# Kernel tuning notes

Measured on AMD Instinct MI355X. Metric: run time of the kernel, lower is better.

The kernel has to match this reference:

```python
import jax, jax.numpy as jnp
import numpy as np

B, S, D, H, HD, F = 2, 2048, 1024, 16, 64, 4096
EPS = 1e-5


def layer_norm(x, g, b):
    m = jnp.mean(x, axis=-1, keepdims=True)
    v = jnp.var(x, axis=-1, keepdims=True)
    return (x - m) * jax.lax.rsqrt(v + EPS) * g + b


def setup_inputs() -> dict:
    key = jax.random.key(0)
    ks = jax.random.split(key, 8)
    hidden_states = jax.random.normal(ks[0], (B, S, D), dtype=jnp.float32)
    # additive causal mask: 0 where allowed, -1e9 where masked
    causal = jnp.tril(jnp.ones((S, S), dtype=bool))
    attention_mask = jnp.where(causal, 0.0, -1e9).astype(jnp.float32)[None, None]
    sd = 1.0 / np.sqrt(D)
    Wq = jax.random.normal(ks[1], (D, D), jnp.float32) * sd
    Wk = jax.random.normal(ks[2], (D, D), jnp.float32) * sd
    Wv = jax.random.normal(ks[3], (D, D), jnp.float32) * sd
    Wo = jax.random.normal(ks[4], (D, D), jnp.float32) * sd
    W1 = jax.random.normal(ks[5], (D, F), jnp.float32) * sd
    W2 = jax.random.normal(ks[6], (F, D), jnp.float32) * (1.0 / np.sqrt(F))
    ln1_g = jnp.ones((D,), jnp.float32)
    ln1_b = jnp.zeros((D,), jnp.float32)
    ln2_g = jnp.ones((D,), jnp.float32)
    ln2_b = jnp.zeros((D,), jnp.float32)
    return dict(hidden_states=hidden_states, attention_mask=attention_mask,
                ln1_g=ln1_g, ln1_b=ln1_b, Wq=Wq, Wk=Wk, Wv=Wv, Wo=Wo,
                ln2_g=ln2_g, ln2_b=ln2_b, W1=W1, W2=W2)


def reference(hidden_states, attention_mask, ln1_g, ln1_b, Wq, Wk, Wv, Wo,
              ln2_g, ln2_b, W1, W2):
    x = hidden_states
    # --- attention sublayer (pre-LN) ---
    h = layer_norm(x, ln1_g, ln1_b)
    q = (h @ Wq).reshape(B, S, H, HD).transpose(0, 2, 1, 3)  # b h s d
    k = (h @ Wk).reshape(B, S, H, HD).transpose(0, 2, 1, 3)
    v = (h @ Wv).reshape(B, S, H, HD).transpose(0, 2, 1, 3)
    scores = jnp.einsum('bhqd,bhkd->bhqk', q, k) / np.sqrt(HD)
    scores = scores + attention_mask
    attn = jax.nn.softmax(scores, axis=-1)
    ctx = jnp.einsum('bhqk,bhkd->bhqd', attn, v)
    ctx = ctx.transpose(0, 2, 1, 3).reshape(B, S, D)
    x = x + ctx @ Wo
    # --- FFN sublayer (pre-LN) ---
    h = layer_norm(x, ln2_g, ln2_b)
    h = jax.nn.gelu(h @ W1, approximate=False) @ W2
    out = x + h
    return out, k, v
```

## Files before the change

### kernel.cpp

```cpp
#include <hip/hip_runtime.h>
#include <hip/hip_bf16.h>
#include <cstdint>
#include <cstddef>

#define BB 2
#define SS 2048
#define DD 1024
#define HH 16
#define HDIM 64
#define FF 4096
#define RR (BB*SS)

typedef __attribute__((ext_vector_type(8))) short short8;
typedef __attribute__((ext_vector_type(4))) float floatx4;

__device__ __forceinline__ unsigned short f2bf(float f){
    __hip_bfloat16 h = __float2bfloat16(f);
    return *reinterpret_cast<unsigned short*>(&h);
}

__device__ __forceinline__ void load_lds16(const void* g, void* l){
    __builtin_amdgcn_global_load_lds((__attribute__((address_space(1))) void*)g,
                                     (__attribute__((address_space(3))) void*)l, 16, 0, 0);
}


template<int BN, int EPI>
__global__ __launch_bounds__(256) void gemm_bt(const unsigned short* __restrict__ A,
                                               const unsigned short* __restrict__ B,
                                               int M, int N, int K, int KS,
                                               float* __restrict__ cf,
                                               const float* __restrict__ resid,
                                               unsigned short* __restrict__ cbf,
                                               unsigned short* __restrict__ qb,
                                               float* __restrict__ kout,
                                               unsigned short* __restrict__ kbf,
                                               float* __restrict__ vout)
{
    constexpr int MI_M = (BN==128) ? 4 : 2;
    __shared__ __align__(16) unsigned short As[2][128*64];
    __shared__ __align__(16) unsigned short Bs[2][BN*64];
    const int tid  = threadIdx.x;
    const int lane = tid & 63;
    const int wave = tid >> 6;
    const int quad = lane >> 4, l15 = lane & 15;
    const int wrow = (BN==128) ? (wave>>1)*64 : wave*32;
    const int wcol = (BN==128) ? (wave&1)*64 : 0;

    const unsigned gx = gridDim.x;
    const unsigned nwg = gx * gridDim.y;
    const unsigned bid = blockIdx.y * gx + blockIdx.x;
    const unsigned cpx = nwg >> 3;
    const unsigned swz = (bid & 7) * cpx + (bid >> 3);
    const int bx = (int)(swz % gx), by = (int)(swz / gx);

    const int gm0 = by * 128, gn0 = bx * BN;
    const int k0 = blockIdx.z * KS;
    const int niter = KS >> 6;
    const int phase = (int)((unsigned)(bx + by) % (unsigned)niter);

    floatx4 acc[MI_M][4];
#pragma unroll
    for (int i=0;i<MI_M;i++)
#pragma unroll
        for (int j=0;j<4;j++) acc[i][j] = (floatx4){0.f,0.f,0.f,0.f};

    const int rsub = lane >> 3;
    const int d8   = (lane & 7) * 8;
    const int ksub = ((lane & 7) ^ rsub) * 8;
    constexpr int nchw = (128 + BN) / 32;

    auto stage = [&](int kt, int buf){
#pragma unroll
        for (int i=0;i<nchw;i++){
            int c = wave*nchw + i;
            if (c < 16)
                load_lds16(A + (size_t)(gm0 + c*8 + rsub)*K + kt + ksub,
                           &As[buf][c*512 + rsub*64 + d8]);
            else
                load_lds16(B + (size_t)(gn0 + (c-16)*8 + rsub)*K + kt + ksub,
                           &Bs[buf][(c-16)*512 + rsub*64 + d8]);
        }
    };

    stage(k0 + phase*64, 0);
    int cur = 0;
    for (int it=0; it<niter; it++){
        __syncthreads();
        if (it+1 < niter){
            int j = it + 1 + phase; if (j >= niter) j -= niter;
            stage(k0 + j*64, cur^1);
        }
        const unsigned short* as = As[cur];
        const unsigned short* bs = Bs[cur];
#pragma unroll
        for (int kk=0; kk<64; kk+=32){
            const int cb4 = kk >> 3;
            short8 af[MI_M], bfr[4];
#pragma unroll
            for (int mi=0;mi<MI_M;mi++){
                int row = wrow + mi*16 + l15;
                af[mi] = *(const short8*)&as[row*64 + (((cb4+quad) ^ (row&7)))*8];
            }
#pragma unroll
            for (int ni=0;ni<4;ni++){
                int row = wcol + ni*16 + l15;
                bfr[ni] = *(const short8*)&bs[row*64 + (((cb4+quad) ^ (row&7)))*8];
            }
#pragma unroll
            for (int mi=0;mi<MI_M;mi++)
#pragma unroll
                for (int ni=0;ni<4;ni++)
                    acc[mi][ni] = __builtin_amdgcn_mfma_f32_16x16x32_bf16(af[mi], bfr[ni], acc[mi][ni], 0, 0, 0);
        }
        cur ^= 1;
    }

#pragma unroll
    for (int mi=0;mi<MI_M;mi++)
#pragma unroll
        for (int ni=0;ni<4;ni++)
#pragma unroll
            for (int r=0;r<4;r++){
                int row = gm0 + wrow + mi*16 + quad*4 + r;
                int col = gn0 + wcol + ni*16 + l15;
                float v = acc[mi][ni][r];
                if constexpr (EPI == 1){
                    int region = gn0 >> 10;
                    if (region == 0){
                        qb[(size_t)row*1024 + col] = f2bf(v);
                    } else {
                        int c1 = col & 1023;
                        int h = c1 >> 6, d = c1 & 63;
                        int b = row >> 11, s = row & (SS-1);
                        size_t o = ((size_t)((b*HH + h)*SS + s))*HDIM + d;
                        if (region == 1){ kout[o] = v; kbf[o] = f2bf(v); }
                        else            { vout[o] = v; }
                    }
                } else if constexpr (EPI == 2){
                    size_t o = (size_t)row*N + col;
                    cf[o] = v + resid[o];
                } else if constexpr (EPI == 3){
                    float u = v*(0.79788456f + 0.0356774081f*v*v);
                    float g = v / (1.f + exp2f(-2.88539008f*u));
                    cbf[(size_t)row*N + col] = f2bf(g);
                } else {
                    cf[(size_t)blockIdx.z*M*N + (size_t)row*N + col] = v;
                }
            }
}

__global__ __launch_bounds__(256) void combine2_kernel(const float* __restrict__ p0,
                                                       const float* __restrict__ p1,
                                                       const float* __restrict__ resid,
                                                       float* __restrict__ out, int n4)
{
    const int i = blockIdx.x*256 + threadIdx.x;
    if (i >= n4) return;
    float4 a = ((const float4*)p0)[i];
    float4 b = ((const float4*)p1)[i];
    float4 c = ((const float4*)resid)[i];
    ((float4*)out)[i] = make_float4(a.x+b.x+c.x, a.y+b.y+c.y, a.z+b.z+c.z, a.w+b.w+c.w);
}

__global__ __launch_bounds__(256) void attn_kernel(const unsigned short* __restrict__ qbf,
                                                   const unsigned short* __restrict__ kbf,
                                                   const unsigned short* __restrict__ vtbf,
                                                   unsigned short* __restrict__ ctx)
{
    __shared__ unsigned short Ks[2][64*64];
    __shared__ unsigned short Vs[2][64*64];
    __shared__ unsigned short Ps[4][16*64];
    const int tid  = threadIdx.x;
    const int lane = tid & 63;
    const int wave = tid >> 6;
    const int quad = lane >> 4, l15 = lane & 15;
    const int aqt = blockIdx.x;
    const int bqt = 31 - aqt;
    const int bh = blockIdx.y;
    const int b = bh >> 4, h = bh & 15;
    const int q0a = aqt * 64, q0b = bqt * 64;

    const unsigned short* kb  = kbf  + (size_t)bh * SS * HDIM;
    const unsigned short* vtb = vtbf + (size_t)bh * HDIM * SS;

    const unsigned short* qra = qbf + (size_t)(b*SS + q0a + wave*16 + l15)*DD + h*HDIM + quad*8;
    const unsigned short* qrb = qbf + (size_t)(b*SS + q0b + wave*16 + l15)*DD + h*HDIM + quad*8;
    short8 qa0 = *(const short8*)qra;
    short8 qa1 = *(const short8*)(qra + 32);
    short8 qb0 = *(const short8*)qrb;
    short8 qb1 = *(const short8*)(qrb + 32);

    float lpA[4] = {0.f,0.f,0.f,0.f}, lpB[4] = {0.f,0.f,0.f,0.f};
    floatx4 accA[4], accB[4];
#pragma unroll
    for (int n=0;n<4;n++){ accA[n] = (floatx4){0.f,0.f,0.f,0.f}; accB[n] = (floatx4){0.f,0.f,0.f,0.f}; }

    const int r8 = lane >> 3;
    const int c8 = ((lane & 7) ^ r8) * 8;
    const int d8 = (lane & 7) * 8;
    const int nkt = bqt + 1;
    const float SC = 0.125f * 1.44269504f;

#pragma unroll
    for (int p=0;p<2;p++){
        int row = p*32 + wave*8 + r8;
        load_lds16(kb  + (size_t)row*HDIM + c8,  &Ks[0][row*64 + d8]);
        load_lds16(vtb + (size_t)row*SS   + c8,  &Vs[0][row*64 + d8]);
    }

    unsigned short* pl = Ps[wave];
    int cur = 0;
    for (int kt=0; kt<nkt; kt++){
        __syncthreads();
        if (kt+1 < nkt){
            int nb = cur ^ 1;
#pragma unroll
            for (int p=0;p<2;p++){
                int row = p*32 + wave*8 + r8;
                load_lds16(kb  + (size_t)((kt+1)*64 + row)*HDIM + c8, &Ks[nb][row*64 + d8]);
                load_lds16(vtb + (size_t)row*SS + (size_t)(kt+1)*64 + c8, &Vs[nb][row*64 + d8]);
            }
        }
        const unsigned short* ks = Ks[cur];
        const unsigned short* vs = Vs[cur];

        short8 kf0[4], kf1[4];
#pragma unroll
        for (int j=0;j<4;j++){
            int row = j*16 + l15;
            kf0[j] = *(const short8*)&ks[row*64 + ((quad     ^ (row&7)))*8];
            kf1[j] = *(const short8*)&ks[row*64 + (((quad+4) ^ (row&7)))*8];
        }
        short8 vf0[4], vf1[4];
#pragma unroll
        for (int n=0;n<4;n++){
            int row = n*16 + l15;
            vf0[n] = *(const short8*)&vs[row*64 + ((quad     ^ (row&7)))*8];
            vf1[n] = *(const short8*)&vs[row*64 + (((quad+4) ^ (row&7)))*8];
        }

        {
            floatx4 s[4];
            __builtin_amdgcn_s_setprio(1);
#pragma unroll
            for (int j=0;j<4;j++){
                floatx4 zz = (floatx4){0.f,0.f,0.f,0.f};
                zz = __builtin_amdgcn_mfma_f32_16x16x32_bf16(qb0, kf0[j], zz, 0, 0, 0);
                zz = __builtin_amdgcn_mfma_f32_16x16x32_bf16(qb1, kf1[j], zz, 0, 0, 0);
                s[j] = zz;
            }
            __builtin_amdgcn_s_setprio(0);
#pragma unroll
            for (int j=0;j<4;j++)
#pragma unroll
                for (int r=0;r<4;r++){
                    int prow = quad*4 + r;
                    float p = exp2f(s[j][r]*SC);
                    if (kt == bqt){
                        int row = q0b + wave*16 + prow;
                        int col = kt*64 + j*16 + l15;
                        if (col > row) p = 0.f;
                    }
                    lpB[r] += p;
                    int ch = (2*j + (l15>>3)) ^ (prow&7);
                    pl[prow*64 + ch*8 + (l15&7)] = f2bf(p);
                }
            short8 pf0 = *(const short8*)&pl[l15*64 + ((quad     ^ (l15&7)))*8];
            short8 pf1 = *(const short8*)&pl[l15*64 + (((quad+4) ^ (l15&7)))*8];
            __builtin_amdgcn_s_setprio(1);
#pragma unroll
            for (int n=0;n<4;n++){
                accB[n] = __builtin_amdgcn_mfma_f32_16x16x32_bf16(pf0, vf0[n], accB[n], 0, 0, 0);
                accB[n] = __builtin_amdgcn_mfma_f32_16x16x32_bf16(pf1, vf1[n], accB[n], 0, 0, 0);
            }
            __builtin_amdgcn_s_setprio(0);
        }

        if (kt <= aqt){
            floatx4 s[4];
            __builtin_amdgcn_s_setprio(1);
#pragma unroll
            for (int j=0;j<4;j++){
                floatx4 zz = (floatx4){0.f,0.f,0.f,0.f};
                zz = __builtin_amdgcn_mfma_f32_16x16x32_bf16(qa0, kf0[j], zz, 0, 0, 0);
                zz = __builtin_amdgcn_mfma_f32_16x16x32_bf16(qa1, kf1[j], zz, 0, 0, 0);
                s[j] = zz;
            }
            __builtin_amdgcn_s_setprio(0);
#pragma unroll
            for (int j=0;j<4;j++)
#pragma unroll
                for (int r=0;r<4;r++){
                    int prow = quad*4 + r;
                    float p = exp2f(s[j][r]*SC);
                    if (kt == aqt){
                        int row = q0a + wave*16 + prow;
                        int col = kt*64 + j*16 + l15;
                        if (col > row) p = 0.f;
                    }
                    lpA[r] += p;
                    int ch = (2*j + (l15>>3)) ^ (prow&7);
                    pl[prow*64 + ch*8 + (l15&7)] = f2bf(p);
                }
            short8 pf0 = *(const short8*)&pl[l15*64 + ((quad     ^ (l15&7)))*8];
            short8 pf1 = *(const short8*)&pl[l15*64 + (((quad+4) ^ (l15&7)))*8];
            __builtin_amdgcn_s_setprio(1);
#pragma unroll
            for (int n=0;n<4;n++){
                accA[n] = __builtin_amdgcn_mfma_f32_16x16x32_bf16(pf0, vf0[n], accA[n], 0, 0, 0);
                accA[n] = __builtin_amdgcn_mfma_f32_16x16x32_bf16(pf1, vf1[n], accA[n], 0, 0, 0);
            }
            __builtin_amdgcn_s_setprio(0);
        }
        cur ^= 1;
    }

#pragma unroll
    for (int r=0;r<4;r++){
        float va = lpA[r], vb = lpB[r];
        va += __shfl_xor(va, 1); vb += __shfl_xor(vb, 1);
        va += __shfl_xor(va, 2); vb += __shfl_xor(vb, 2);
        va += __shfl_xor(va, 4); vb += __shfl_xor(vb, 4);
        va += __shfl_xor(va, 8); vb += __shfl_xor(vb, 8);
        lpA[r] = va; lpB[r] = vb;
    }
#pragma unroll
    for (int n=0;n<4;n++)
#pragma unroll
        for (int r=0;r<4;r++){
            float oa = accA[n][r] / lpA[r];
            float ob = accB[n][r] / lpB[r];
            ctx[(size_t)(b*SS + q0a + wave*16 + quad*4 + r)*DD + h*HDIM + n*16 + l15] = f2bf(oa);
            ctx[(size_t)(b*SS + q0b + wave*16 + quad*4 + r)*DD + h*HDIM + n*16 + l15] = f2bf(ob);
        }
}

__global__ __launch_bounds__(256) void ln_kernel(const float* __restrict__ x,
                                                 const float* __restrict__ g,
                                                 const float* __restrict__ bparm,
                                                 unsigned short* __restrict__ out)
{
    __shared__ float red[8];
    const int row = blockIdx.x;
    const int tid = threadIdx.x;
    const float* xr = x + (size_t)row*DD;
    float4 v = *(const float4*)(xr + tid*4);
    float s  = v.x+v.y+v.z+v.w;
    float sq = v.x*v.x + v.y*v.y + v.z*v.z + v.w*v.w;
#pragma unroll
    for (int off=1; off<64; off<<=1){ s += __shfl_xor(s, off); sq += __shfl_xor(sq, off); }
    if ((tid & 63) == 0){ red[tid>>6] = s; red[4 + (tid>>6)] = sq; }
    __syncthreads();
    float ts = red[0]+red[1]+red[2]+red[3];
    float tq = red[4]+red[5]+red[6]+red[7];
    float mean = ts * (1.f/DD);
    float var  = tq * (1.f/DD) - mean*mean;
    float inv  = rsqrtf(var + 1e-5f);
    float4 gv = *(const float4*)(g + tid*4);
    float4 bv = *(const float4*)(bparm + tid*4);
    ushort4 o;
    o.x = f2bf((v.x-mean)*inv*gv.x + bv.x);
    o.y = f2bf((v.y-mean)*inv*gv.y + bv.y);
    o.z = f2bf((v.z-mean)*inv*gv.z + bv.z);
    o.w = f2bf((v.w-mean)*inv*gv.w + bv.w);
    *(ushort4*)(out + (size_t)row*DD + tid*4) = o;
}

__global__ __launch_bounds__(256) void castT_kernel(const float* __restrict__ in,
                                                    unsigned short* __restrict__ out,
                                                    int R, int C)
{
    __shared__ float t[32][33];
    const size_t zoff = (size_t)blockIdx.z * R * C;
    in  += zoff; out += zoff;
    const int tr = blockIdx.y*32, tc = blockIdx.x*32;
    const int lr = threadIdx.x >> 5, lc = threadIdx.x & 31;
#pragma unroll
    for (int i=0;i<4;i++)
        t[lr + i*8][lc] = in[(size_t)(tr + lr + i*8)*C + tc + lc];
    __syncthreads();
#pragma unroll
    for (int i=0;i<4;i++)
        out[(size_t)(tc + lr + i*8)*R + tr + lc] = f2bf(t[lc][lr + i*8]);
}

__global__ __launch_bounds__(256) void castT4_kernel(const float* __restrict__ i0,
                                                     const float* __restrict__ i1,
                                                     const float* __restrict__ i2,
                                                     const float* __restrict__ i3,
                                                     unsigned short* __restrict__ o0,
                                                     unsigned short* __restrict__ o1,
                                                     unsigned short* __restrict__ o2,
                                                     unsigned short* __restrict__ o3)
{
    __shared__ float t[32][33];
    const int z = blockIdx.z;
    const float* in = (z==0) ? i0 : (z==1) ? i1 : (z==2) ? i2 : i3;
    unsigned short* out = (z==0) ? o0 : (z==1) ? o1 : (z==2) ? o2 : o3;
    const int tr = blockIdx.y*32, tc = blockIdx.x*32;
    const int lr = threadIdx.x >> 5, lc = threadIdx.x & 31;
#pragma unroll
    for (int i=0;i<4;i++)
        t[lr + i*8][lc] = in[(size_t)(tr + lr + i*8)*1024 + tc + lc];
    __syncthreads();
#pragma unroll
    for (int i=0;i<4;i++)
        out[(size_t)(tc + lr + i*8)*1024 + tr + lc] = f2bf(t[lc][lr + i*8]);
}

extern "C" void kernel_launch(void* const* d_in, const int* in_sizes, int n_in,
                              void* d_out, int out_size, void* d_ws, size_t ws_size,
                              hipStream_t stream)
{
    const float* x     = (const float*)d_in[0];
    const float* ln1_g = (const float*)d_in[2];
    const float* ln1_b = (const float*)d_in[3];
    const float* Wq    = (const float*)d_in[4];
    const float* Wk    = (const float*)d_in[5];
    const float* Wv    = (const float*)d_in[6];
    const float* Wo    = (const float*)d_in[7];
    const float* ln2_g = (const float*)d_in[8];
    const float* ln2_b = (const float*)d_in[9];
    const float* W1    = (const float*)d_in[10];
    const float* W2    = (const float*)d_in[11];

    float* out  = (float*)d_out;
    float* kout = out  + (size_t)RR*DD;
    float* vout = kout + (size_t)BB*HH*SS*HDIM;

    char* w = (char*)d_ws;
    auto alloc = [&](size_t bytes) -> char* {
        char* p = w; w += (bytes + 255) & ~(size_t)255; return p;
    };
    unsigned short* qkvT  = (unsigned short*)alloc((size_t)3072*1024*2);
    unsigned short* WoT   = (unsigned short*)alloc((size_t)1024*1024*2);
    unsigned short* W1T   = (unsigned short*)alloc((size_t)4096*1024*2);
    unsigned short* W2T   = (unsigned short*)alloc((size_t)1024*4096*2);
    unsigned short* h_bf  = (unsigned short*)alloc((size_t)RR*DD*2);
    unsigned short* q_bf  = (unsigned short*)alloc((size_t)RR*DD*2);
    unsigned short* k_bf  = (unsigned short*)alloc((size_t)RR*DD*2);
    unsigned short* vt_bf = (unsigned short*)alloc((size_t)RR*DD*2);
    unsigned short* ctx_bf= (unsigned short*)alloc((size_t)RR*DD*2);
    unsigned short* act_bf= (unsigned short*)alloc((size_t)RR*FF*2);
    float* x1     = (float*)alloc((size_t)RR*DD*4);
    float* fpart  = (float*)alloc((size_t)2*RR*DD*4);

    castT4_kernel<<<dim3(32,32,4), 256, 0, stream>>>(
        Wq, Wk, Wv, Wo, qkvT, qkvT + 1024*1024, qkvT + 2*1024*1024, WoT);
    castT_kernel<<<dim3(128,32,1), 256, 0, stream>>>(W1, W1T, 1024, 4096);
    castT_kernel<<<dim3(32,128,1), 256, 0, stream>>>(W2, W2T, 4096, 1024);

    ln_kernel<<<RR, 256, 0, stream>>>(x, ln1_g, ln1_b, h_bf);
    gemm_bt<128,1><<<dim3(3072/128, RR/128), 256, 0, stream>>>(
        h_bf, qkvT, RR, 3072, 1024, 1024, nullptr, nullptr, nullptr, q_bf, kout, k_bf, vout);
    castT_kernel<<<dim3(2, 64, BB*HH), 256, 0, stream>>>(vout, vt_bf, SS, HDIM);
    attn_kernel<<<dim3(16, BB*HH), 256, 0, stream>>>(q_bf, k_bf, vt_bf, ctx_bf);
    gemm_bt<64,2><<<dim3(1024/64, RR/128), 256, 0, stream>>>(
        ctx_bf, WoT, RR, 1024, 1024, 1024, x1, x, nullptr, nullptr, nullptr, nullptr, nullptr);

    ln_kernel<<<RR, 256, 0, stream>>>(x1, ln2_g, ln2_b, h_bf);
    gemm_bt<128,3><<<dim3(4096/128, RR/128), 256, 0, stream>>>(
        h_bf, W1T, RR, 4096, 1024, 1024, nullptr, nullptr, act_bf, nullptr, nullptr, nullptr, nullptr);
    gemm_bt<128,4><<<dim3(1024/128, RR/128, 2), 256, 0, stream>>>(
        act_bf, W2T, RR, 1024, 4096, 2048, fpart, nullptr, nullptr, nullptr, nullptr, nullptr, nullptr);
    combine2_kernel<<<(RR*DD/4 + 255)/256, 256, 0, stream>>>(
        fpart, fpart + (size_t)RR*DD, x1, out, RR*DD/4);
}
```

Baseline: 376.8 us.

## Add triple-buffered LDS pipeline for Wo GEMM and drop attention setprio

Adds an NBUF=3 template path to the bf16 GEMM. It prefetches two K-tiles ahead, uses explicit vmcnt waits in place of a full __syncthreads, and needs only one barrier per iteration. Only the Wo projection GEMM (BN=64) uses it, which should hide more global-to-LDS latency for that small-grid GEMM. The change also removes the s_setprio hints around the MFMA blocks in the attention kernel. Risks are more LDS per block, which lowers occupancy, and correctness depending on the hand-counted vmcnt values matching the number of loads issued per stage.

```diff
diff --git a/kernel.cpp b/kernel.cpp
--- a/kernel.cpp
+++ b/kernel.cpp
@@ -25,7 +25,7 @@
 }
 
 
-template<int BN, int EPI>
+template<int BN, int EPI, int NBUF = 2>
 __global__ __launch_bounds__(256) void gemm_bt(const unsigned short* __restrict__ A,
                                                const unsigned short* __restrict__ B,
                                                int M, int N, int K, int KS,
@@ -38,8 +38,8 @@
                                                float* __restrict__ vout)
 {
     constexpr int MI_M = (BN==128) ? 4 : 2;
-    __shared__ __align__(16) unsigned short As[2][128*64];
-    __shared__ __align__(16) unsigned short Bs[2][BN*64];
+    __shared__ __align__(16) unsigned short As[NBUF][128*64];
+    __shared__ __align__(16) unsigned short Bs[NBUF][BN*64];
     const int tid  = threadIdx.x;
     const int lane = tid & 63;
     const int wave = tid >> 6;
@@ -83,16 +83,7 @@
         }
     };
 
-    stage(k0 + phase*64, 0);
-    int cur = 0;
-    for (int it=0; it<niter; it++){
-        __syncthreads();
-        if (it+1 < niter){
-            int j = it + 1 + phase; if (j >= niter) j -= niter;
-            stage(k0 + j*64, cur^1);
-        }
-        const unsigned short* as = As[cur];
-        const unsigned short* bs = Bs[cur];
+    auto compute = [&](const unsigned short* as, const unsigned short* bs){
 #pragma unroll
         for (int kk=0; kk<64; kk+=32){
             const int cb4 = kk >> 3;
@@ -113,7 +104,45 @@
                 for (int ni=0;ni<4;ni++)
                     acc[mi][ni] = __builtin_amdgcn_mfma_f32_16x16x32_bf16(af[mi], bfr[ni], acc[mi][ni], 0, 0, 0);
         }
-        cur ^= 1;
+    };
+
+    if constexpr (NBUF == 2){
+        stage(k0 + phase*64, 0);
+        int cur = 0;
+        for (int it=0; it<niter; it++){
+            __syncthreads();
+            if (it+1 < niter){
+                int j = it + 1 + phase; if (j >= niter) j -= niter;
+                stage(k0 + j*64, cur^1);
+            }
+            compute(As[cur], Bs[cur]);
+            cur ^= 1;
+        }
+    } else {
+        stage(k0 + phase*64, 0);
+        if (niter > 1){
+            int j1 = 1 + phase; if (j1 >= niter) j1 -= niter;
+            stage(k0 + j1*64, 1);
+        }
+        int cur = 0;
+        for (int it=0; it<niter; it++){
+            if (it+1 < niter){
+                if constexpr (nchw == 6) asm volatile("s_waitcnt vmcnt(6)" ::: "memory");
+                else                     asm volatile("s_waitcnt vmcnt(8)" ::: "memory");
+            } else {
+                asm volatile("s_waitcnt vmcnt(0)" ::: "memory");
+            }
+            __builtin_amdgcn_s_barrier();
+            asm volatile("" ::: "memory");
+            if (it+2 < niter){
+                int j = it + 2 + phase;
+                if (j >= niter) j -= niter;
+                if (j >= niter) j -= niter;
+                stage(k0 + j*64, (cur+2)%3);
+            }
+            compute(As[cur], Bs[cur]);
+            cur = (cur+1)%3;
+        }
     }
 
 #pragma unroll
@@ -242,7 +271,6 @@
 
         {
             floatx4 s[4];
-            __builtin_amdgcn_s_setprio(1);
 #pragma unroll
             for (int j=0;j<4;j++){
                 floatx4 zz = (floatx4){0.f,0.f,0.f,0.f};
@@ -250,7 +278,6 @@
                 zz = __builtin_amdgcn_mfma_f32_16x16x32_bf16(qb1, kf1[j], zz, 0, 0, 0);
                 s[j] = zz;
             }
-            __builtin_amdgcn_s_setprio(0);
 #pragma unroll
             for (int j=0;j<4;j++)
 #pragma unroll
@@ -268,18 +295,15 @@
                 }
             short8 pf0 = *(const short8*)&pl[l15*64 + ((quad     ^ (l15&7)))*8];
             short8 pf1 = *(const short8*)&pl[l15*64 + (((quad+4) ^ (l15&7)))*8];
-            __builtin_amdgcn_s_setprio(1);
 #pragma unroll
             for (int n=0;n<4;n++){
                 accB[n] = __builtin_amdgcn_mfma_f32_16x16x32_bf16(pf0, vf0[n], accB[n], 0, 0, 0);
                 accB[n] = __builtin_amdgcn_mfma_f32_16x16x32_bf16(pf1, vf1[n], accB[n], 0, 0, 0);
             }
-            __builtin_amdgcn_s_setprio(0);
         }
 
         if (kt <= aqt){
             floatx4 s[4];
-            __builtin_amdgcn_s_setprio(1);
 #pragma unroll
             for (int j=0;j<4;j++){
                 floatx4 zz = (floatx4){0.f,0.f,0.f,0.f};
@@ -287,7 +311,6 @@
                 zz = __builtin_amdgcn_mfma_f32_16x16x32_bf16(qa1, kf1[j], zz, 0, 0, 0);
                 s[j] = zz;
             }
-            __builtin_amdgcn_s_setprio(0);
 #pragma unroll
             for (int j=0;j<4;j++)
 #pragma unroll
@@ -305,13 +328,11 @@
                 }
             short8 pf0 = *(const short8*)&pl[l15*64 + ((quad     ^ (l15&7)))*8];
             short8 pf1 = *(const short8*)&pl[l15*64 + (((quad+4) ^ (l15&7)))*8];
-            __builtin_amdgcn_s_setprio(1);
 #pragma unroll
             for (int n=0;n<4;n++){
                 accA[n] = __builtin_amdgcn_mfma_f32_16x16x32_bf16(pf0, vf0[n], accA[n], 0, 0, 0);
                 accA[n] = __builtin_amdgcn_mfma_f32_16x16x32_bf16(pf1, vf1[n], accA[n], 0, 0, 0);
             }
-            __builtin_amdgcn_s_setprio(0);
         }
         cur ^= 1;
     }
@@ -456,7 +477,7 @@
         h_bf, qkvT, RR, 3072, 1024, 1024, nullptr, nullptr, nullptr, q_bf, kout, k_bf, vout);
     castT_kernel<<<dim3(2, 64, BB*HH), 256, 0, stream>>>(vout, vt_bf, SS, HDIM);
     attn_kernel<<<dim3(16, BB*HH), 256, 0, stream>>>(q_bf, k_bf, vt_bf, ctx_bf);
-    gemm_bt<64,2><<<dim3(1024/64, RR/128), 256, 0, stream>>>(
+    gemm_bt<64,2,3><<<dim3(1024/64, RR/128), 256, 0, stream>>>(
         ctx_bf, WoT, RR, 1024, 1024, 1024, x1, x, nullptr, nullptr, nullptr, nullptr, nullptr);
 
     ln_kernel<<<RR, 256, 0, stream>>>(x1, ln2_g, ln2_b, h_bf);
```

Result: no change. 376.0 us (-0.2%).

## Switch GEMMs to single-buffered LDS with higher occupancy; drop attention setprio

Applied to the files above, without the earlier changes.

Adds an NBUF template parameter to the GEMM. All launches now use a single LDS buffer with stage/sync/compute/sync per K step instead of double-buffered prefetch, and launch_bounds requests 3 workgroups per CU. The goal is to halve LDS usage so more workgroups fit per CU and hide latency across workgroups instead of within one. It also removes the s_setprio hints around the MFMA blocks in the attention kernel. The cost is that in-block load/compute overlap is lost and an extra barrier is added per iteration.

```diff
diff --git a/kernel.cpp b/kernel.cpp
--- a/kernel.cpp
+++ b/kernel.cpp
@@ -25,21 +25,21 @@
 }
 
 
-template<int BN, int EPI>
-__global__ __launch_bounds__(256) void gemm_bt(const unsigned short* __restrict__ A,
-                                               const unsigned short* __restrict__ B,
-                                               int M, int N, int K, int KS,
-                                               float* __restrict__ cf,
-                                               const float* __restrict__ resid,
-                                               unsigned short* __restrict__ cbf,
-                                               unsigned short* __restrict__ qb,
-                                               float* __restrict__ kout,
-                                               unsigned short* __restrict__ kbf,
-                                               float* __restrict__ vout)
+template<int BN, int EPI, int NBUF = 1>
+__global__ __launch_bounds__(256, 3) void gemm_bt(const unsigned short* __restrict__ A,
+                                                  const unsigned short* __restrict__ B,
+                                                  int M, int N, int K, int KS,
+                                                  float* __restrict__ cf,
+                                                  const float* __restrict__ resid,
+                                                  unsigned short* __restrict__ cbf,
+                                                  unsigned short* __restrict__ qb,
+                                                  float* __restrict__ kout,
+                                                  unsigned short* __restrict__ kbf,
+                                                  float* __restrict__ vout)
 {
     constexpr int MI_M = (BN==128) ? 4 : 2;
-    __shared__ __align__(16) unsigned short As[2][128*64];
-    __shared__ __align__(16) unsigned short Bs[2][BN*64];
+    __shared__ __align__(16) unsigned short As[NBUF][128*64];
+    __shared__ __align__(16) unsigned short Bs[NBUF][BN*64];
     const int tid  = threadIdx.x;
     const int lane = tid & 63;
     const int wave = tid >> 6;
@@ -83,16 +83,7 @@
         }
     };
 
-    stage(k0 + phase*64, 0);
-    int cur = 0;
-    for (int it=0; it<niter; it++){
-        __syncthreads();
-        if (it+1 < niter){
-            int j = it + 1 + phase; if (j >= niter) j -= niter;
-            stage(k0 + j*64, cur^1);
-        }
-        const unsigned short* as = As[cur];
-        const unsigned short* bs = Bs[cur];
+    auto compute = [&](const unsigned short* as, const unsigned short* bs){
 #pragma unroll
         for (int kk=0; kk<64; kk+=32){
             const int cb4 = kk >> 3;
@@ -113,7 +104,28 @@
                 for (int ni=0;ni<4;ni++)
                     acc[mi][ni] = __builtin_amdgcn_mfma_f32_16x16x32_bf16(af[mi], bfr[ni], acc[mi][ni], 0, 0, 0);
         }
-        cur ^= 1;
+    };
+
+    if constexpr (NBUF == 1){
+        for (int it=0; it<niter; it++){
+            int j = it + phase; if (j >= niter) j -= niter;
+            stage(k0 + j*64, 0);
+            __syncthreads();
+            compute(As[0], Bs[0]);
+            __syncthreads();
+        }
+    } else {
+        stage(k0 + phase*64, 0);
+        int cur = 0;
+        for (int it=0; it<niter; it++){
+            __syncthreads();
+            if (it+1 < niter){
+                int j = it + 1 + phase; if (j >= niter) j -= niter;
+                stage(k0 + j*64, cur^1);
+            }
+            compute(As[cur], Bs[cur]);
+            cur ^= 1;
+        }
     }
 
 #pragma unroll
@@ -242,7 +254,6 @@
 
         {
             floatx4 s[4];
-            __builtin_amdgcn_s_setprio(1);
 #pragma unroll
             for (int j=0;j<4;j++){
                 floatx4 zz = (floatx4){0.f,0.f,0.f,0.f};
@@ -250,7 +261,6 @@
                 zz = __builtin_amdgcn_mfma_f32_16x16x32_bf16(qb1, kf1[j], zz, 0, 0, 0);
                 s[j] = zz;
             }
-            __builtin_amdgcn_s_setprio(0);
 #pragma unroll
             for (int j=0;j<4;j++)
 #pragma unroll
@@ -268,18 +278,15 @@
                 }
             short8 pf0 = *(const short8*)&pl[l15*64 + ((quad     ^ (l15&7)))*8];
             short8 pf1 = *(const short8*)&pl[l15*64 + (((quad+4) ^ (l15&7)))*8];
-            __builtin_amdgcn_s_setprio(1);
 #pragma unroll
             for (int n=0;n<4;n++){
                 accB[n] = __builtin_amdgcn_mfma_f32_16x16x32_bf16(pf0, vf0[n], accB[n], 0, 0, 0);
                 accB[n] = __builtin_amdgcn_mfma_f32_16x16x32_bf16(pf1, vf1[n], accB[n], 0, 0, 0);
             }
-            __builtin_amdgcn_s_setprio(0);
         }
 
         if (kt <= aqt){
             floatx4 s[4];
-            __builtin_amdgcn_s_setprio(1);
 #pragma unroll
             for (int j=0;j<4;j++){
                 floatx4 zz = (floatx4){0.f,0.f,0.f,0.f};
@@ -287,7 +294,6 @@
                 zz = __builtin_amdgcn_mfma_f32_16x16x32_bf16(qa1, kf1[j], zz, 0, 0, 0);
                 s[j] = zz;
             }
-            __builtin_amdgcn_s_setprio(0);
 #pragma unroll
             for (int j=0;j<4;j++)
 #pragma unroll
@@ -305,13 +311,11 @@
                 }
             short8 pf0 = *(const short8*)&pl[l15*64 + ((quad     ^ (l15&7)))*8];
             short8 pf1 = *(const short8*)&pl[l15*64 + (((quad+4) ^ (l15&7)))*8];
-            __builtin_amdgcn_s_setprio(1);
 #pragma unroll
             for (int n=0;n<4;n++){
                 accA[n] = __builtin_amdgcn_mfma_f32_16x16x32_bf16(pf0, vf0[n], accA[n], 0, 0, 0);
                 accA[n] = __builtin_amdgcn_mfma_f32_16x16x32_bf16(pf1, vf1[n], accA[n], 0, 0, 0);
             }
-            __builtin_amdgcn_s_setprio(0);
         }
         cur ^= 1;
     }
@@ -452,17 +456,17 @@
     castT_kernel<<<dim3(32,128,1), 256, 0, stream>>>(W2, W2T, 4096, 1024);
 
     ln_kernel<<<RR, 256, 0, stream>>>(x, ln1_g, ln1_b, h_bf);
-    gemm_bt<128,1><<<dim3(3072/128, RR/128), 256, 0, stream>>>(
+    gemm_bt<128,1,1><<<dim3(3072/128, RR/128), 256, 0, stream>>>(
         h_bf, qkvT, RR, 3072, 1024, 1024, nullptr, nullptr, nullptr, q_bf, kout, k_bf, vout);
     castT_kernel<<<dim3(2, 64, BB*HH), 256, 0, stream>>>(vout, vt_bf, SS, HDIM);
     attn_kernel<<<dim3(16, BB*HH), 256, 0, stream>>>(q_bf, k_bf, vt_bf, ctx_bf);
-    gemm_bt<64,2><<<dim3(1024/64, RR/128), 256, 0, stream>>>(
+    gemm_bt<64,2,1><<<dim3(1024/64, RR/128), 256, 0, stream>>>(
         ctx_bf, WoT, RR, 1024, 1024, 1024, x1, x, nullptr, nullptr, nullptr, nullptr, nullptr);
 
     ln_kernel<<<RR, 256, 0, stream>>>(x1, ln2_g, ln2_b, h_bf);
-    gemm_bt<128,3><<<dim3(4096/128, RR/128), 256, 0, stream>>>(
+    gemm_bt<128,3,1><<<dim3(4096/128, RR/128), 256, 0, stream>>>(
         h_bf, W1T, RR, 4096, 1024, 1024, nullptr, nullptr, act_bf, nullptr, nullptr, nullptr, nullptr);
-    gemm_bt<128,4><<<dim3(1024/128, RR/128, 2), 256, 0, stream>>>(
+    gemm_bt<128,4,1><<<dim3(1024/128, RR/128, 2), 256, 0, stream>>>(
         act_bf, W2T, RR, 1024, 4096, 2048, fpart, nullptr, nullptr, nullptr, nullptr, nullptr, nullptr);
     combine2_kernel<<<(RR*DD/4 + 255)/256, 256, 0, stream>>>(
         fpart, fpart + (size_t)RR*DD, x1, out, RR*DD/4);
```

Measured after the change: 365.1 us. -3.1%, faster.
